# Performance work log

Hardware: AMD Instinct MI355X
Metric: run time of the kernel (lower is better)

Reference implementation:

```python
import jax, jax.numpy as jnp
import numpy as np


def _unfold(x, k):
    """x: [B, C, Hp, Wp] -> patches [B, C, H, W, k, k] (stride 1)."""
    H = x.shape[2] - k + 1
    W = x.shape[3] - k + 1
    rows = [jnp.stack([x[:, :, i:i + H, j:j + W] for j in range(k)], axis=-1)
            for i in range(k)]
    return jnp.stack(rows, axis=-2)  # [B,C,H,W,k,k]


def _gconv1x1(x, w):
    """Grouped 1x1 conv. x: [B,C,H,W], w: [g, out_g, in_g] -> [B,g,out_g,H,W]."""
    B, C, H, W = x.shape
    g, og, ig = w.shape
    xg = x.reshape(B, g, ig, H, W)
    return jnp.einsum('bgihw,goi->bgohw', xg, w)


def setup_inputs() -> dict:
    key = jax.random.key(0)
    ks = jax.random.split(key, 6)
    B, Cin, H, W = 4, 64, 96, 96
    Cout, g, k = 64, 8, 7
    og, ig = Cout // g, Cin // g
    fan_scale = (2.0 / Cout) ** 0.5  # kaiming-like scale for 1x1 conv
    return {
        'x': jax.random.normal(ks[0], (B, Cin, H, W), jnp.float32),
        'wq': jax.random.normal(ks[1], (g, og, ig), jnp.float32) * fan_scale,
        'wk': jax.random.normal(ks[2], (g, og, ig), jnp.float32) * fan_scale,
        'wv': jax.random.normal(ks[3], (g, og, ig), jnp.float32) * fan_scale,
        'h_emb': jax.random.normal(ks[4], (g, og // 2, k), jnp.float32),
        'w_emb': jax.random.normal(ks[5], (g, og // 2, k), jnp.float32),
    }


def reference(x, wq, wk, wv, h_emb, w_emb):
    B, C, H, W = x.shape
    g, og, _ = wq.shape
    k = h_emb.shape[-1]
    pad = (k - 1) // 2  # stride=1, padding=(k-1)//2 per module config
    xp = jnp.pad(x, ((0, 0), (0, 0), (pad, pad), (pad, pad)))

    q = _gconv1x1(x, wq)                                   # [B,g,og,H,W]
    k_full = _gconv1x1(xp, wk).reshape(B, C, H + 2 * pad, W + 2 * pad)
    v_full = _gconv1x1(xp, wv).reshape(B, C, H + 2 * pad, W + 2 * pad)

    k_unf = _unfold(k_full, k).reshape(B, g, og, H, W, k * k)
    v_unf = _unfold(v_full, k).reshape(B, g, og, H, W, k * k)

    # relative position embedding: top half channels vary along patch rows,
    # bottom half along patch cols -> [g, og, k*k]
    h_part = jnp.broadcast_to(h_emb[:, :, :, None], (g, og // 2, k, k))
    w_part = jnp.broadcast_to(w_emb[:, :, None, :], (g, og // 2, k, k))
    emb = jnp.concatenate([h_part, w_part], axis=1).reshape(g, og, k * k)

    logits = q[..., None] * (k_unf + emb[None, :, :, None, None, :])
    att = jax.nn.softmax(logits, axis=-1)                  # [B,g,og,H,W,k^2]
    out = jnp.einsum('bgchwk,bgchwk->bgchw', att, v_unf)
    return out.reshape(B, C, H, W)
```

## Files before the change

kernel.cpp:

```cpp
#include <hip/hip_runtime.h>


constexpr int Bc = 4, Cc = 64, Hc = 96, Wc = 96;
constexpr int G = 8, OG = 8, IG = 8, KK = 7, PAD = 3;
constexpr int TH = 32, TW = 16;
constexpr int SH = TH + KK - 1;
constexpr int SWD = TW + KK - 1;
constexpr int SW2 = 25;
constexpr int TILES_H = Hc / TH, TILES_W = Wc / TW;
constexpr int TILES = TILES_H * TILES_W;
constexpr int PLANE = Hc * Wc;
constexpr int OCB = 2;
constexpr int NB = Bc * G * 4 * TILES;
constexpr float LOG2E = 1.4426950408889634f;

#define OC_LOOP(HALFC)                                                            \
  _Pragma("unroll 1")                                                             \
  for (int oc = 0; oc < OCB; ++oc) {                                              \
    const float qv0 = qvs[oc][0], qv1 = qvs[oc][1];                               \
    float qe0[KK], qe1[KK];                                                       \
    _Pragma("unroll")                                                             \
    for (int t = 0; t < KK; ++t) {                                                \
      const float e = eb[oc * KK + t];                                            \
      qe0[t] = qv0 * e; qe1[t] = qv1 * e;                                         \
    }                                                                             \
    float s0a = 0.f, s0b = 0.f, o0a = 0.f, o0b = 0.f;                             \
    float s1a = 0.f, s1b = 0.f, o1a = 0.f, o1b = 0.f;                             \
    const float2* rp = &kvs[oc][r0][tx];                                          \
    _Pragma("unroll")                                                             \
    for (int i = 0; i < 8; ++i) {                                                 \
      float2 row[KK];                                                             \
      _Pragma("unroll")                                                           \
      for (int j = 0; j < KK; ++j) row[j] = rp[i * SW2 + j];                      \
      if (i < 7) {                                                                \
        _Pragma("unroll")                                                         \
        for (int j = 0; j < KK; ++j) {                                            \
          const float ev = __builtin_amdgcn_exp2f(                                \
              fmaf(qv0, row[j].x, (HALFC) ? qe0[j] : qe0[i]));                    \
          if (j & 1) { s0b += ev; o0b = fmaf(ev, row[j].y, o0b); }                \
          else       { s0a += ev; o0a = fmaf(ev, row[j].y, o0a); }                \
        }                                                                         \
      }                                                                           \
      if (i >= 1) {                                                               \
        _Pragma("unroll")                                                         \
        for (int j = 0; j < KK; ++j) {                                            \
          const float ev = __builtin_amdgcn_exp2f(                                \
              fmaf(qv1, row[j].x, (HALFC) ? qe1[j] : qe1[i - 1]));                \
          if (j & 1) { s1b += ev; o1b = fmaf(ev, row[j].y, o1b); }                \
          else       { s1a += ev; o1a = fmaf(ev, row[j].y, o1a); }                \
        }                                                                         \
      }                                                                           \
    }                                                                             \
    ob[oc * PLANE]      = (o0a + o0b) * __builtin_amdgcn_rcpf(s0a + s0b);         \
    ob[oc * PLANE + Wc] = (o1a + o1b) * __builtin_amdgcn_rcpf(s1a + s1b);         \
  }

__global__ __launch_bounds__(256, 8)
void sasa_kernel(const float* __restrict__ x,
                 const float* __restrict__ wq,
                 const float* __restrict__ wk,
                 const float* __restrict__ wv,
                 const float* __restrict__ h_emb,
                 const float* __restrict__ w_emb,
                 float* __restrict__ out)
{
    __shared__ float2 kvs[OCB][SH][SW2];

    const int tid = threadIdx.x;
    const int L = (blockIdx.x & 7) * (NB / 8) + (blockIdx.x >> 3);
    const int tile    = L % TILES;
    const int rest    = L / TILES;
    const int quarter = rest & 3;
    const int gi      = (rest >> 2) & 7;
    const int b       = rest >> 5;
    const int half    = quarter >> 1;
    const int th0     = (tile / TILES_W) * TH;
    const int tw0     = (tile % TILES_W) * TW;

    const float* xb  = x  + (size_t)(b * Cc + gi * IG) * PLANE;
    const float* wqg = wq + gi * OG * IG + quarter * OCB * IG;
    const float* wkg = wk + gi * OG * IG + quarter * OCB * IG;
    const float* wvg = wv + gi * OG * IG + quarter * OCB * IG;
    const float* eb  = (half ? w_emb : h_emb) + gi * (OG / 2) * KK
                                              + (quarter & 1) * OCB * KK;

    const int tx  = tid & 15;
    const int r0  = 2 * (tid >> 4);
    const int h0  = th0 + r0;
    const int wg  = tw0 + tx;
    float xc0[IG], xc1[IG];
    {
        const float* xp = xb + (size_t)h0 * Wc + wg;
        #pragma unroll
        for (int i = 0; i < IG; ++i) {
            xc0[i] = xp[i * PLANE];
            xc1[i] = xp[i * PLANE + Wc];
        }
    }

    for (int e = tid; e < SH * SWD; e += 256) {
        const int hy = e / SWD, hx = e - hy * SWD;
        const int gy = th0 + hy - PAD;
        const int gx = tw0 + hx - PAD;
        const bool valid = ((unsigned)gy < (unsigned)Hc) && ((unsigned)gx < (unsigned)Wc);
        float xv[IG];
        #pragma unroll
        for (int i = 0; i < IG; ++i)
            xv[i] = valid ? xb[i * PLANE + gy * Wc + gx] : 0.0f;
        #pragma unroll
        for (int oc = 0; oc < OCB; ++oc) {
            float ka = 0.f, va = 0.f;
            #pragma unroll
            for (int i = 0; i < IG; ++i) {
                ka = fmaf(xv[i], wkg[oc * IG + i], ka);
                va = fmaf(xv[i], wvg[oc * IG + i], va);
            }
            kvs[oc][hy][hx] = make_float2(ka, va);
        }
    }

    float qvs[OCB][2];
    #pragma unroll
    for (int oc = 0; oc < OCB; ++oc) {
        float q0 = 0.f, q1 = 0.f;
        #pragma unroll
        for (int i = 0; i < IG; ++i) {
            const float wqi = wqg[oc * IG + i];
            q0 = fmaf(xc0[i], wqi, q0);
            q1 = fmaf(xc1[i], wqi, q1);
        }
        qvs[oc][0] = q0 * LOG2E;
        qvs[oc][1] = q1 * LOG2E;
    }
    __syncthreads();

    float* ob = out + (size_t)(b * Cc + gi * OG + quarter * OCB) * PLANE
                    + (size_t)h0 * Wc + wg;

    if (half == 0) { OC_LOOP(0) } else { OC_LOOP(1) }
}

extern "C" void kernel_launch(void* const* d_in, const int* in_sizes, int n_in,
                              void* d_out, int out_size, void* d_ws, size_t ws_size,
                              hipStream_t stream)
{
    const float* x     = (const float*)d_in[0];
    const float* wq    = (const float*)d_in[1];
    const float* wk    = (const float*)d_in[2];
    const float* wv    = (const float*)d_in[3];
    const float* h_emb = (const float*)d_in[4];
    const float* w_emb = (const float*)d_in[5];
    float* out = (float*)d_out;

    sasa_kernel<<<NB, 256, 0, stream>>>(x, wq, wk, wv, h_emb, w_emb, out);
}
```

Baseline: 28.57 us.

## Compute 2x2 outputs per thread with wider 32x32 tiles for K/V reuse

```diff
diff --git a/kernel.cpp b/kernel.cpp
--- a/kernel.cpp
+++ b/kernel.cpp
@@ -3,10 +3,10 @@
 
 constexpr int Bc = 4, Cc = 64, Hc = 96, Wc = 96;
 constexpr int G = 8, OG = 8, IG = 8, KK = 7, PAD = 3;
-constexpr int TH = 32, TW = 16;
+constexpr int TH = 32, TW = 32;
 constexpr int SH = TH + KK - 1;
 constexpr int SWD = TW + KK - 1;
-constexpr int SW2 = 25;
+constexpr int SW2 = 39;
 constexpr int TILES_H = Hc / TH, TILES_W = Wc / TW;
 constexpr int TILES = TILES_H * TILES_W;
 constexpr int PLANE = Hc * Wc;
@@ -14,48 +14,65 @@
 constexpr int NB = Bc * G * 4 * TILES;
 constexpr float LOG2E = 1.4426950408889634f;
 
-#define OC_LOOP(HALFC)                                                            \
-  _Pragma("unroll 1")                                                             \
-  for (int oc = 0; oc < OCB; ++oc) {                                              \
-    const float qv0 = qvs[oc][0], qv1 = qvs[oc][1];                               \
-    float qe0[KK], qe1[KK];                                                       \
-    _Pragma("unroll")                                                             \
-    for (int t = 0; t < KK; ++t) {                                                \
-      const float e = eb[oc * KK + t];                                            \
-      qe0[t] = qv0 * e; qe1[t] = qv1 * e;                                         \
-    }                                                                             \
-    float s0a = 0.f, s0b = 0.f, o0a = 0.f, o0b = 0.f;                             \
-    float s1a = 0.f, s1b = 0.f, o1a = 0.f, o1b = 0.f;                             \
-    const float2* rp = &kvs[oc][r0][tx];                                          \
-    _Pragma("unroll")                                                             \
-    for (int i = 0; i < 8; ++i) {                                                 \
-      float2 row[KK];                                                             \
-      _Pragma("unroll")                                                           \
-      for (int j = 0; j < KK; ++j) row[j] = rp[i * SW2 + j];                      \
-      if (i < 7) {                                                                \
-        _Pragma("unroll")                                                         \
-        for (int j = 0; j < KK; ++j) {                                            \
-          const float ev = __builtin_amdgcn_exp2f(                                \
-              fmaf(qv0, row[j].x, (HALFC) ? qe0[j] : qe0[i]));                    \
-          if (j & 1) { s0b += ev; o0b = fmaf(ev, row[j].y, o0b); }                \
-          else       { s0a += ev; o0a = fmaf(ev, row[j].y, o0a); }                \
-        }                                                                         \
-      }                                                                           \
-      if (i >= 1) {                                                               \
-        _Pragma("unroll")                                                         \
-        for (int j = 0; j < KK; ++j) {                                            \
-          const float ev = __builtin_amdgcn_exp2f(                                \
-              fmaf(qv1, row[j].x, (HALFC) ? qe1[j] : qe1[i - 1]));                \
-          if (j & 1) { s1b += ev; o1b = fmaf(ev, row[j].y, o1b); }                \
-          else       { s1a += ev; o1a = fmaf(ev, row[j].y, o1a); }                \
-        }                                                                         \
-      }                                                                           \
-    }                                                                             \
-    ob[oc * PLANE]      = (o0a + o0b) * __builtin_amdgcn_rcpf(s0a + s0b);         \
-    ob[oc * PLANE + Wc] = (o1a + o1b) * __builtin_amdgcn_rcpf(s1a + s1b);         \
+#define OC_LOOP(HALFC)                                                             \
+  _Pragma("unroll 1")                                                              \
+  for (int oc = 0; oc < OCB; ++oc) {                                               \
+    const float qv00 = qvs[oc][0], qv01 = qvs[oc][1];                              \
+    const float qv10 = qvs[oc][2], qv11 = qvs[oc][3];                              \
+    float qe00[KK], qe01[KK], qe10[KK], qe11[KK];                                  \
+    _Pragma("unroll")                                                              \
+    for (int t = 0; t < KK; ++t) {                                                 \
+      const float e = eb[oc * KK + t];                                             \
+      qe00[t] = qv00 * e; qe01[t] = qv01 * e;                                      \
+      qe10[t] = qv10 * e; qe11[t] = qv11 * e;                                      \
+    }                                                                              \
+    float s00a=0.f,s00b=0.f,o00a=0.f,o00b=0.f;                                     \
+    float s01a=0.f,s01b=0.f,o01a=0.f,o01b=0.f;                                     \
+    float s10a=0.f,s10b=0.f,o10a=0.f,o10b=0.f;                                     \
+    float s11a=0.f,s11b=0.f,o11a=0.f,o11b=0.f;                                     \
+    const float2* rp = &kvs[oc][r0][c0];                                           \
+    _Pragma("unroll")                                                              \
+    for (int i = 0; i < 8; ++i) {                                                  \
+      float2 row[8];                                                               \
+      _Pragma("unroll")                                                            \
+      for (int jj = 0; jj < 8; ++jj) row[jj] = rp[i * SW2 + jj];                   \
+      if (i < 7) {                                                                 \
+        _Pragma("unroll")                                                          \
+        for (int j = 0; j < KK; ++j) {                                             \
+          const float e0 = __builtin_amdgcn_exp2f(                                 \
+              fmaf(qv00, row[j].x,     (HALFC) ? qe00[j] : qe00[i]));              \
+          const float e1 = __builtin_amdgcn_exp2f(                                 \
+              fmaf(qv01, row[j + 1].x, (HALFC) ? qe01[j] : qe01[i]));              \
+          if (j & 1) { s00b += e0; o00b = fmaf(e0, row[j].y,     o00b);            \
+                       s01b += e1; o01b = fmaf(e1, row[j + 1].y, o01b); }          \
+          else       { s00a += e0; o00a = fmaf(e0, row[j].y,     o00a);            \
+                       s01a += e1; o01a = fmaf(e1, row[j + 1].y, o01a); }          \
+        }                                                                          \
+      }                                                                            \
+      if (i >= 1) {                                                                \
+        _Pragma("unroll")                                                          \
+        for (int j = 0; j < KK; ++j) {                                             \
+          const float e0 = __builtin_amdgcn_exp2f(                                 \
+              fmaf(qv10, row[j].x,     (HALFC) ? qe10[j] : qe10[i - 1]));          \
+          const float e1 = __builtin_amdgcn_exp2f(                                 \
+              fmaf(qv11, row[j + 1].x, (HALFC) ? qe11[j] : qe11[i - 1]));          \
+          if (j & 1) { s10b += e0; o10b = fmaf(e0, row[j].y,     o10b);            \
+                       s11b += e1; o11b = fmaf(e1, row[j + 1].y, o11b); }          \
+          else       { s10a += e0; o10a = fmaf(e0, row[j].y,     o10a);            \
+                       s11a += e1; o11a = fmaf(e1, row[j + 1].y, o11a); }          \
+        }                                                                          \
+      }                                                                            \
+    }                                                                              \
+    float2 r0v, r1v;                                                               \
+    r0v.x = (o00a + o00b) * __builtin_amdgcn_rcpf(s00a + s00b);                    \
+    r0v.y = (o01a + o01b) * __builtin_amdgcn_rcpf(s01a + s01b);                    \
+    r1v.x = (o10a + o10b) * __builtin_amdgcn_rcpf(s10a + s10b);                    \
+    r1v.y = (o11a + o11b) * __builtin_amdgcn_rcpf(s11a + s11b);                    \
+    *(float2*)(ob + oc * PLANE)      = r0v;                                        \
+    *(float2*)(ob + oc * PLANE + Wc) = r1v;                                        \
   }
 
-__global__ __launch_bounds__(256, 8)
+__global__ __launch_bounds__(256, 4)
 void sasa_kernel(const float* __restrict__ x,
                  const float* __restrict__ wq,
                  const float* __restrict__ wk,
@@ -84,17 +101,18 @@
     const float* eb  = (half ? w_emb : h_emb) + gi * (OG / 2) * KK
                                               + (quarter & 1) * OCB * KK;
 
-    const int tx  = tid & 15;
-    const int r0  = 2 * (tid >> 4);
-    const int h0  = th0 + r0;
-    const int wg  = tw0 + tx;
-    float xc0[IG], xc1[IG];
+    const int tx = tid & 15;
+    const int r0 = 2 * (tid >> 4);
+    const int c0 = 2 * tx;
+    const int h0 = th0 + r0;
+    const int w0 = tw0 + c0;
+    float2 xr0[IG], xr1[IG];
     {
-        const float* xp = xb + (size_t)h0 * Wc + wg;
+        const float* xp = xb + (size_t)h0 * Wc + w0;
         #pragma unroll
         for (int i = 0; i < IG; ++i) {
-            xc0[i] = xp[i * PLANE];
-            xc1[i] = xp[i * PLANE + Wc];
+            xr0[i] = *(const float2*)(xp + i * PLANE);
+            xr1[i] = *(const float2*)(xp + i * PLANE + Wc);
         }
     }
 
@@ -119,23 +137,27 @@
         }
     }
 
-    float qvs[OCB][2];
+    float qvs[OCB][4];
     #pragma unroll
     for (int oc = 0; oc < OCB; ++oc) {
-        float q0 = 0.f, q1 = 0.f;
+        float q00 = 0.f, q01 = 0.f, q10 = 0.f, q11 = 0.f;
         #pragma unroll
         for (int i = 0; i < IG; ++i) {
             const float wqi = wqg[oc * IG + i];
-            q0 = fmaf(xc0[i], wqi, q0);
-            q1 = fmaf(xc1[i], wqi, q1);
+            q00 = fmaf(xr0[i].x, wqi, q00);
+            q01 = fmaf(xr0[i].y, wqi, q01);
+            q10 = fmaf(xr1[i].x, wqi, q10);
+            q11 = fmaf(xr1[i].y, wqi, q11);
         }
-        qvs[oc][0] = q0 * LOG2E;
-        qvs[oc][1] = q1 * LOG2E;
+        qvs[oc][0] = q00 * LOG2E;
+        qvs[oc][1] = q01 * LOG2E;
+        qvs[oc][2] = q10 * LOG2E;
+        qvs[oc][3] = q11 * LOG2E;
     }
     __syncthreads();
 
     float* ob = out + (size_t)(b * Cc + gi * OG + quarter * OCB) * PLANE
-                    + (size_t)h0 * Wc + wg;
+                    + (size_t)h0 * Wc + w0;
 
     if (half == 0) { OC_LOOP(0) } else { OC_LOOP(1) }
 }
```

Result: slower. 49.71 us (+74.0%).

## Split QKV projection into a separate kernel writing padded K/V and Q to workspace

Applied to the files above, without the earlier changes.

```diff
diff --git a/kernel.cpp b/kernel.cpp
--- a/kernel.cpp
+++ b/kernel.cpp
@@ -3,6 +3,8 @@
 
 constexpr int Bc = 4, Cc = 64, Hc = 96, Wc = 96;
 constexpr int G = 8, OG = 8, IG = 8, KK = 7, PAD = 3;
+constexpr int HP = 102, WPS = 104;
+constexpr int KVPLANE = HP * WPS;
 constexpr int TH = 32, TW = 16;
 constexpr int SH = TH + KK - 1;
 constexpr int SWD = TW + KK - 1;
@@ -13,6 +15,49 @@
 constexpr int OCB = 2;
 constexpr int NB = Bc * G * 4 * TILES;
 constexpr float LOG2E = 1.4426950408889634f;
+
+__global__ __launch_bounds__(256)
+void qkv_kernel(const float* __restrict__ x,
+                const float* __restrict__ wq,
+                const float* __restrict__ wk,
+                const float* __restrict__ wv,
+                float2* __restrict__ kv,
+                float* __restrict__ q)
+{
+    const int bg = blockIdx.y;
+    const int gi = bg & 7, b = bg >> 3;
+    const int p  = blockIdx.x * 256 + threadIdx.x;
+    if (p >= HP * HP) return;
+    const int hp = p / HP, wp = p % HP;
+    const int gy = hp - PAD, gx = wp - PAD;
+    const bool valid = ((unsigned)gy < (unsigned)Hc) && ((unsigned)gx < (unsigned)Wc);
+
+    const float* xb  = x  + (size_t)(b * Cc + gi * IG) * PLANE;
+    const float* wqg = wq + gi * OG * IG;
+    const float* wkg = wk + gi * OG * IG;
+    const float* wvg = wv + gi * OG * IG;
+
+    float xv[IG];
+    #pragma unroll
+    for (int i = 0; i < IG; ++i)
+        xv[i] = valid ? xb[i * PLANE + gy * Wc + gx] : 0.0f;
+
+    float2* kvb = kv + (size_t)(bg * OG) * KVPLANE + hp * WPS + wp;
+    float*  qb  = q  + (size_t)(b * Cc + gi * OG) * PLANE + gy * Wc + gx;
+
+    #pragma unroll
+    for (int oc = 0; oc < OG; ++oc) {
+        float ka = 0.f, va = 0.f, qa = 0.f;
+        #pragma unroll
+        for (int i = 0; i < IG; ++i) {
+            ka = fmaf(xv[i], wkg[oc * IG + i], ka);
+            va = fmaf(xv[i], wvg[oc * IG + i], va);
+            qa = fmaf(xv[i], wqg[oc * IG + i], qa);
+        }
+        kvb[(size_t)oc * KVPLANE] = make_float2(ka, va);
+        if (valid) qb[(size_t)oc * PLANE] = qa;
+    }
+}
 
 #define OC_LOOP(HALFC)                                                            \
   _Pragma("unroll 1")                                                             \
@@ -56,10 +101,8 @@
   }
 
 __global__ __launch_bounds__(256, 8)
-void sasa_kernel(const float* __restrict__ x,
-                 const float* __restrict__ wq,
-                 const float* __restrict__ wk,
-                 const float* __restrict__ wv,
+void attn_kernel(const float2* __restrict__ kv,
+                 const float* __restrict__ q,
                  const float* __restrict__ h_emb,
                  const float* __restrict__ w_emb,
                  float* __restrict__ out)
@@ -77,60 +120,31 @@
     const int th0     = (tile / TILES_W) * TH;
     const int tw0     = (tile % TILES_W) * TW;
 
-    const float* xb  = x  + (size_t)(b * Cc + gi * IG) * PLANE;
-    const float* wqg = wq + gi * OG * IG + quarter * OCB * IG;
-    const float* wkg = wk + gi * OG * IG + quarter * OCB * IG;
-    const float* wvg = wv + gi * OG * IG + quarter * OCB * IG;
-    const float* eb  = (half ? w_emb : h_emb) + gi * (OG / 2) * KK
-                                              + (quarter & 1) * OCB * KK;
+    const float* eb = (half ? w_emb : h_emb) + gi * (OG / 2) * KK
+                                             + (quarter & 1) * OCB * KK;
 
-    const int tx  = tid & 15;
-    const int r0  = 2 * (tid >> 4);
-    const int h0  = th0 + r0;
-    const int wg  = tw0 + tx;
-    float xc0[IG], xc1[IG];
+    const int tx = tid & 15;
+    const int r0 = 2 * (tid >> 4);
+    const int h0 = th0 + r0;
+    const int wg = tw0 + tx;
+
+    float qvs[OCB][2];
     {
-        const float* xp = xb + (size_t)h0 * Wc + wg;
+        const float* qp = q + (size_t)(b * Cc + gi * OG + quarter * OCB) * PLANE
+                            + (size_t)h0 * Wc + wg;
         #pragma unroll
-        for (int i = 0; i < IG; ++i) {
-            xc0[i] = xp[i * PLANE];
-            xc1[i] = xp[i * PLANE + Wc];
+        for (int oc = 0; oc < OCB; ++oc) {
+            qvs[oc][0] = qp[oc * PLANE] * LOG2E;
+            qvs[oc][1] = qp[oc * PLANE + Wc] * LOG2E;
         }
     }
 
-    for (int e = tid; e < SH * SWD; e += 256) {
-        const int hy = e / SWD, hx = e - hy * SWD;
-        const int gy = th0 + hy - PAD;
-        const int gx = tw0 + hx - PAD;
-        const bool valid = ((unsigned)gy < (unsigned)Hc) && ((unsigned)gx < (unsigned)Wc);
-        float xv[IG];
-        #pragma unroll
-        for (int i = 0; i < IG; ++i)
-            xv[i] = valid ? xb[i * PLANE + gy * Wc + gx] : 0.0f;
-        #pragma unroll
-        for (int oc = 0; oc < OCB; ++oc) {
-            float ka = 0.f, va = 0.f;
-            #pragma unroll
-            for (int i = 0; i < IG; ++i) {
-                ka = fmaf(xv[i], wkg[oc * IG + i], ka);
-                va = fmaf(xv[i], wvg[oc * IG + i], va);
-            }
-            kvs[oc][hy][hx] = make_float2(ka, va);
-        }
-    }
-
-    float qvs[OCB][2];
-    #pragma unroll
-    for (int oc = 0; oc < OCB; ++oc) {
-        float q0 = 0.f, q1 = 0.f;
-        #pragma unroll
-        for (int i = 0; i < IG; ++i) {
-            const float wqi = wqg[oc * IG + i];
-            q0 = fmaf(xc0[i], wqi, q0);
-            q1 = fmaf(xc1[i], wqi, q1);
-        }
-        qvs[oc][0] = q0 * LOG2E;
-        qvs[oc][1] = q1 * LOG2E;
+    const float2* kvg = kv + (size_t)((b * G + gi) * OG + quarter * OCB) * KVPLANE;
+    for (int e = tid; e < 2 * SH * SWD; e += 256) {
+        const int oc = e / (SH * SWD);
+        const int r  = e - oc * (SH * SWD);
+        const int hy = r / SWD, hx = r - hy * SWD;
+        kvs[oc][hy][hx] = kvg[(size_t)oc * KVPLANE + (th0 + hy) * WPS + (tw0 + hx)];
     }
     __syncthreads();
 
@@ -152,5 +166,10 @@
     const float* w_emb = (const float*)d_in[5];
     float* out = (float*)d_out;
 
-    sasa_kernel<<<NB, 256, 0, stream>>>(x, wq, wk, wv, h_emb, w_emb, out);
+    float2* kv = (float2*)d_ws;
+    float*  qb = (float*)((char*)d_ws + (size_t)Bc * G * OG * KVPLANE * sizeof(float2));
+
+    dim3 gridA((HP * HP + 255) / 256, Bc * G);
+    qkv_kernel<<<gridA, 256, 0, stream>>>(x, wq, wk, wv, kv, qb);
+    attn_kernel<<<NB, 256, 0, stream>>>(kv, qb, h_emb, w_emb, out);
 }
```

Result: slower. 40.19 us (+40.7%).

## Interleave both output channels into float4 LDS layout and process them jointly

Applied to the files above, without the earlier changes.

```diff
diff --git a/kernel.cpp b/kernel.cpp
--- a/kernel.cpp
+++ b/kernel.cpp
@@ -6,7 +6,7 @@
 constexpr int TH = 32, TW = 16;
 constexpr int SH = TH + KK - 1;
 constexpr int SWD = TW + KK - 1;
-constexpr int SW2 = 25;
+constexpr int SW4 = 23;
 constexpr int TILES_H = Hc / TH, TILES_W = Wc / TW;
 constexpr int TILES = TILES_H * TILES_W;
 constexpr int PLANE = Hc * Wc;
@@ -14,48 +14,53 @@
 constexpr int NB = Bc * G * 4 * TILES;
 constexpr float LOG2E = 1.4426950408889634f;
 
-#define OC_LOOP(HALFC)                                                            \
-  _Pragma("unroll 1")                                                             \
-  for (int oc = 0; oc < OCB; ++oc) {                                              \
-    const float qv0 = qvs[oc][0], qv1 = qvs[oc][1];                               \
-    float qe0[KK], qe1[KK];                                                       \
-    _Pragma("unroll")                                                             \
-    for (int t = 0; t < KK; ++t) {                                                \
-      const float e = eb[oc * KK + t];                                            \
-      qe0[t] = qv0 * e; qe1[t] = qv1 * e;                                         \
-    }                                                                             \
-    float s0a = 0.f, s0b = 0.f, o0a = 0.f, o0b = 0.f;                             \
-    float s1a = 0.f, s1b = 0.f, o1a = 0.f, o1b = 0.f;                             \
-    const float2* rp = &kvs[oc][r0][tx];                                          \
+#define PHASE2(HALFC)                                                             \
+  {                                                                               \
+    float sa[2][2] = {{0.f,0.f},{0.f,0.f}}, sb[2][2] = {{0.f,0.f},{0.f,0.f}};     \
+    float oa[2][2] = {{0.f,0.f},{0.f,0.f}}, obv[2][2] = {{0.f,0.f},{0.f,0.f}};    \
+    const float4* rp = &kvs[r0][tx];                                              \
     _Pragma("unroll")                                                             \
     for (int i = 0; i < 8; ++i) {                                                 \
-      float2 row[KK];                                                             \
+      float4 row[8];                                                              \
       _Pragma("unroll")                                                           \
-      for (int j = 0; j < KK; ++j) row[j] = rp[i * SW2 + j];                      \
+      for (int jj = 0; jj < 8; ++jj) row[jj] = rp[i * SW4 + jj];                  \
       if (i < 7) {                                                                \
         _Pragma("unroll")                                                         \
         for (int j = 0; j < KK; ++j) {                                            \
-          const float ev = __builtin_amdgcn_exp2f(                                \
-              fmaf(qv0, row[j].x, (HALFC) ? qe0[j] : qe0[i]));                    \
-          if (j & 1) { s0b += ev; o0b = fmaf(ev, row[j].y, o0b); }                \
-          else       { s0a += ev; o0a = fmaf(ev, row[j].y, o0a); }                \
+          const float ev0 = __builtin_amdgcn_exp2f(                               \
+              fmaf(qv[0][0], row[j].x, qe[0][0][(HALFC) ? j : i]));               \
+          const float ev1 = __builtin_amdgcn_exp2f(                               \
+              fmaf(qv[1][0], row[j].z, qe[1][0][(HALFC) ? j : i]));               \
+          if (j & 1) { sb[0][0] += ev0; obv[0][0] = fmaf(ev0, row[j].y, obv[0][0]);\
+                       sb[1][0] += ev1; obv[1][0] = fmaf(ev1, row[j].w, obv[1][0]);}\
+          else       { sa[0][0] += ev0; oa[0][0] = fmaf(ev0, row[j].y, oa[0][0]); \
+                       sa[1][0] += ev1; oa[1][0] = fmaf(ev1, row[j].w, oa[1][0]);}\
         }                                                                         \
       }                                                                           \
       if (i >= 1) {                                                               \
         _Pragma("unroll")                                                         \
         for (int j = 0; j < KK; ++j) {                                            \
-          const float ev = __builtin_amdgcn_exp2f(                                \
-              fmaf(qv1, row[j].x, (HALFC) ? qe1[j] : qe1[i - 1]));                \
-          if (j & 1) { s1b += ev; o1b = fmaf(ev, row[j].y, o1b); }                \
-          else       { s1a += ev; o1a = fmaf(ev, row[j].y, o1a); }                \
+          const float ev0 = __builtin_amdgcn_exp2f(                               \
+              fmaf(qv[0][1], row[j].x, qe[0][1][(HALFC) ? j : (i - 1)]));         \
+          const float ev1 = __builtin_amdgcn_exp2f(                               \
+              fmaf(qv[1][1], row[j].z, qe[1][1][(HALFC) ? j : (i - 1)]));         \
+          if (j & 1) { sb[0][1] += ev0; obv[0][1] = fmaf(ev0, row[j].y, obv[0][1]);\
+                       sb[1][1] += ev1; obv[1][1] = fmaf(ev1, row[j].w, obv[1][1]);}\
+          else       { sa[0][1] += ev0; oa[0][1] = fmaf(ev0, row[j].y, oa[0][1]); \
+                       sa[1][1] += ev1; oa[1][1] = fmaf(ev1, row[j].w, oa[1][1]);}\
         }                                                                         \
       }                                                                           \
     }                                                                             \
-    ob[oc * PLANE]      = (o0a + o0b) * __builtin_amdgcn_rcpf(s0a + s0b);         \
-    ob[oc * PLANE + Wc] = (o1a + o1b) * __builtin_amdgcn_rcpf(s1a + s1b);         \
+    _Pragma("unroll")                                                             \
+    for (int oc = 0; oc < OCB; ++oc) {                                            \
+      ob[oc * PLANE]      = (oa[oc][0] + obv[oc][0])                              \
+                            * __builtin_amdgcn_rcpf(sa[oc][0] + sb[oc][0]);       \
+      ob[oc * PLANE + Wc] = (oa[oc][1] + obv[oc][1])                              \
+                            * __builtin_amdgcn_rcpf(sa[oc][1] + sb[oc][1]);       \
+    }                                                                             \
   }
 
-__global__ __launch_bounds__(256, 8)
+__global__ __launch_bounds__(256)
 void sasa_kernel(const float* __restrict__ x,
                  const float* __restrict__ wq,
                  const float* __restrict__ wk,
@@ -64,7 +69,7 @@
                  const float* __restrict__ w_emb,
                  float* __restrict__ out)
 {
-    __shared__ float2 kvs[OCB][SH][SW2];
+    __shared__ float4 kvs[SH][SW4];
 
     const int tid = threadIdx.x;
     const int L = (blockIdx.x & 7) * (NB / 8) + (blockIdx.x >> 3);
@@ -84,10 +89,10 @@
     const float* eb  = (half ? w_emb : h_emb) + gi * (OG / 2) * KK
                                               + (quarter & 1) * OCB * KK;
 
-    const int tx  = tid & 15;
-    const int r0  = 2 * (tid >> 4);
-    const int h0  = th0 + r0;
-    const int wg  = tw0 + tx;
+    const int tx = tid & 15;
+    const int r0 = 2 * (tid >> 4);
+    const int h0 = th0 + r0;
+    const int wg = tw0 + tx;
     float xc0[IG], xc1[IG];
     {
         const float* xp = xb + (size_t)h0 * Wc + wg;
@@ -107,19 +112,18 @@
         #pragma unroll
         for (int i = 0; i < IG; ++i)
             xv[i] = valid ? xb[i * PLANE + gy * Wc + gx] : 0.0f;
+        float k0 = 0.f, v0 = 0.f, k1 = 0.f, v1 = 0.f;
         #pragma unroll
-        for (int oc = 0; oc < OCB; ++oc) {
-            float ka = 0.f, va = 0.f;
-            #pragma unroll
-            for (int i = 0; i < IG; ++i) {
-                ka = fmaf(xv[i], wkg[oc * IG + i], ka);
-                va = fmaf(xv[i], wvg[oc * IG + i], va);
-            }
-            kvs[oc][hy][hx] = make_float2(ka, va);
+        for (int i = 0; i < IG; ++i) {
+            k0 = fmaf(xv[i], wkg[i],      k0);
+            v0 = fmaf(xv[i], wvg[i],      v0);
+            k1 = fmaf(xv[i], wkg[IG + i], k1);
+            v1 = fmaf(xv[i], wvg[IG + i], v1);
         }
+        kvs[hy][hx] = make_float4(k0, v0, k1, v1);
     }
 
-    float qvs[OCB][2];
+    float qv[2][2];
     #pragma unroll
     for (int oc = 0; oc < OCB; ++oc) {
         float q0 = 0.f, q1 = 0.f;
@@ -129,15 +133,24 @@
             q0 = fmaf(xc0[i], wqi, q0);
             q1 = fmaf(xc1[i], wqi, q1);
         }
-        qvs[oc][0] = q0 * LOG2E;
-        qvs[oc][1] = q1 * LOG2E;
+        qv[oc][0] = q0 * LOG2E;
+        qv[oc][1] = q1 * LOG2E;
     }
+    float qe[2][2][KK];
+    #pragma unroll
+    for (int oc = 0; oc < OCB; ++oc)
+        #pragma unroll
+        for (int t = 0; t < KK; ++t) {
+            const float e = eb[oc * KK + t];
+            qe[oc][0][t] = qv[oc][0] * e;
+            qe[oc][1][t] = qv[oc][1] * e;
+        }
     __syncthreads();
 
     float* ob = out + (size_t)(b * Cc + gi * OG + quarter * OCB) * PLANE
                     + (size_t)h0 * Wc + wg;
 
-    if (half == 0) { OC_LOOP(0) } else { OC_LOOP(1) }
+    if (half == 0) { PHASE2(0) } else { PHASE2(1) }
 }
 
 extern "C" void kernel_launch(void* const* d_in, const int* in_sizes, int n_in,
```

Result: slower. 36.16 us (+26.6%).
